# Kernel optimization log

Hardware: AMD Instinct MI355X
Metric: run time of the kernel (lower is better)

## Reference

```python
import jax, jax.numpy as jnp
import numpy as np

N = 8192        # nodes
D_IN = 512      # input features
H = 256         # hidden (GAT out_features)
D_OUT = 16      # output classes
K = 16          # num clusters/classes
LRELU_SLOPE = 0.2
MASK_FILL = -9e15
EDGE_P = 0.002  # sparsity of random adjacency


def setup_inputs() -> dict:
    key = jax.random.key(0)
    k1, k2, k3, k4, k5, k6 = jax.random.split(key, 6)
    x = jax.random.normal(k1, (N, D_IN), dtype=jnp.float32)
    # binary adjacency with self loops (module only tests adj > 0; support reused as propagation matrix)
    adj = (jax.random.uniform(k2, (N, N)) < EDGE_P).astype(jnp.float32)
    adj = jnp.maximum(adj, jnp.eye(N, dtype=jnp.float32))
    C_a = jax.random.normal(k3, (K, H), dtype=jnp.float32)
    # learned parameters (xavier-ish scale)
    W = jax.random.normal(k4, (D_IN, H), dtype=jnp.float32) * (1.414 * (2.0 / (D_IN + H)) ** 0.5)
    a = jax.random.normal(k5, (2 * H, 1), dtype=jnp.float32) * (1.414 * (2.0 / (2 * H + 1)) ** 0.5)
    W_gcn = jax.random.normal(k6, (H, D_OUT), dtype=jnp.float32)
    return {"x": x, "adj": adj, "C_a": C_a, "W": W, "a": a, "W_gcn": W_gcn}


def _clust_score(Z, C):
    # score[n,k] = exp(-||Z_n - C_k||) normalized over k (beta = 1)
    d = jnp.sqrt(((Z[:, None, :] - C[None, :, :]) ** 2).sum(-1))  # [N,K]
    s = jnp.exp(-d) + 1e-10
    return s / s.sum(axis=1, keepdims=True)


def reference(x, adj, C_a, W, a, W_gcn):
    h = W.shape[1]
    # --- GAT layer ---
    Wh = x @ W                                   # [N,H]
    Wh1 = Wh @ a[:h, :]                          # [N,1]
    Wh2 = Wh @ a[h:, :]                          # [N,1]
    e = jax.nn.leaky_relu(Wh1 + Wh2.T, LRELU_SLOPE)   # [N,N]
    att = jax.nn.softmax(jnp.where(adj > 0, e, MASK_FILL), axis=1)
    Z_0 = att @ Wh                               # h_prime, [N,H]
    gatoutput = jax.nn.elu(Z_0)
    # --- cluster score on detached Z_0 (update=False path) ---
    score = _clust_score(jax.lax.stop_gradient(Z_0), C_a)
    # --- GCN layer (B_1 = I, so Z_1 = F_1) ---
    F_1 = jax.nn.relu(adj @ (gatoutput @ W_gcn))  # [N,D_OUT]
    output = F_1
    Z_1 = F_1
    return (output, Z_1, Z_0, score)
```

## Files before the change

### kernel.cpp

```cpp
#include <hip/hip_runtime.h>
#include <hip/hip_bf16.h>

#define N_NODES 8192
#define D_IN    512
#define H       256
#define D_OUT   16
#define K_CL    16
#define MAXN    96

#define OUT_OFF 0
#define Z1_OFF  131072
#define Z0_OFF  262144
#define SC_OFF  2359296

typedef unsigned int   u32;
typedef unsigned short u16;
typedef short s16x8 __attribute__((ext_vector_type(8)));
typedef float f32x4 __attribute__((ext_vector_type(4)));

__device__ __forceinline__ float load_in(const void* p, int bf, size_t idx) {
    if (bf) { u32 w = ((const u16*)p)[idx]; return __uint_as_float(w << 16); }
    return ((const float*)p)[idx];
}
__device__ __forceinline__ void store_out(void* p, int bf, size_t idx, float v) {
    if (bf) ((__hip_bfloat16*)p)[idx] = __float2bfloat16(v);
    else    ((float*)p)[idx] = v;
}
__device__ __forceinline__ u16 f2bf(float v) {
    return (u16)__hip_bfloat16_raw(__float2bfloat16(v)).x;
}
__device__ __forceinline__ float bf2f(u16 b) { return __uint_as_float(((u32)b) << 16); }

__global__ void k_detect(const u32* __restrict__ adjw, int* __restrict__ flag) {
    int t = blockIdx.x * 256 + threadIdx.x;
    int hit = 0;
    #pragma unroll 4
    for (int i = 0; i < 64; i++)
        if (adjw[(size_t)t + (size_t)i * 16384] == 0x00003F80u) hit = 1;
    if (hit) atomicOr(flag, 1);
}

__global__ void k_prep(const void* av, const void* C_a, const void* Wgcn, const void* W,
                       const int* __restrict__ flag,
                       float* a_f, float* Ca_f, float* Wg_f,
                       u16* Wht, u16* Wlt) {
    int bf = *flag;
    int i = blockIdx.x * 256 + threadIdx.x;
    if (i < 512)        a_f[i]         = load_in(av,   bf, i);
    else if (i < 4608)  Ca_f[i - 512]  = load_in(C_a,  bf, i - 512);
    else if (i < 8704)  Wg_f[i - 4608] = load_in(Wgcn, bf, i - 4608);
    else if (i < 139776) {
        int j = i - 8704;
        int nn = j >> 9, kk = j & 511;
        size_t src = (size_t)kk * H + nn;
        if (bf) {
            Wht[j] = ((const u16*)W)[src];
            Wlt[j] = 0;
        } else {
            float w = ((const float*)W)[src];
            u16 hi = f2bf(w);
            Wht[j] = hi;
            Wlt[j] = f2bf(w - bf2f(hi));
        }
    }
}

__global__ __launch_bounds__(1024) void k_gemm_wh(
    const void* __restrict__ xraw,
    const u16* __restrict__ Wht, const u16* __restrict__ Wlt,
    const int* __restrict__ flag, float* __restrict__ Wh)
{
    int bf = *flag;
    int tid = threadIdx.x, wave = tid >> 6, lane = tid & 63;
    int m0 = blockIdx.x * 16, n0 = wave * 16;
    int quad = lane >> 4, lr = lane & 15;

    size_t boff = (size_t)(n0 + lr) * D_IN + quad * 8;
    const u16* bh = Wht + boff;
    f32x4 acc = {0.f, 0.f, 0.f, 0.f};

    if (bf) {
        const u16* ah = (const u16*)xraw + (size_t)(m0 + lr) * D_IN + quad * 8;
        #pragma unroll
        for (int k0 = 0; k0 < D_IN; k0 += 32) {
            s16x8 a = *(const s16x8*)(ah + k0);
            s16x8 b = *(const s16x8*)(bh + k0);
            acc = __builtin_amdgcn_mfma_f32_16x16x32_bf16(a, b, acc, 0, 0, 0);
        }
    } else {
        const float* af = (const float*)xraw + (size_t)(m0 + lr) * D_IN + quad * 8;
        const u16* bl = Wlt + boff;
        #pragma unroll
        for (int k0 = 0; k0 < D_IN; k0 += 32) {
            float4 f0 = *(const float4*)(af + k0);
            float4 f1 = *(const float4*)(af + k0 + 4);
            float v[8] = {f0.x, f0.y, f0.z, f0.w, f1.x, f1.y, f1.z, f1.w};
            s16x8 ahi, alo;
            #pragma unroll
            for (int i = 0; i < 8; i++) {
                u16 h = f2bf(v[i]);
                ahi[i] = (short)h;
                alo[i] = (short)f2bf(v[i] - bf2f(h));
            }
            s16x8 b  = *(const s16x8*)(bh + k0);
            s16x8 b2 = *(const s16x8*)(bl + k0);
            acc = __builtin_amdgcn_mfma_f32_16x16x32_bf16(ahi, b,  acc, 0, 0, 0);
            acc = __builtin_amdgcn_mfma_f32_16x16x32_bf16(ahi, b2, acc, 0, 0, 0);
            acc = __builtin_amdgcn_mfma_f32_16x16x32_bf16(alo, b,  acc, 0, 0, 0);
        }
    }
    float* cp = Wh + (size_t)(m0 + quad * 4) * H + n0 + lr;
    #pragma unroll
    for (int i = 0; i < 4; i++) cp[(size_t)i * H] = acc[i];
}

__global__ __launch_bounds__(256) void k_wh12(
    const float* __restrict__ Wh, const float* __restrict__ a_f,
    float* __restrict__ Wh1, float* __restrict__ Wh2)
{
    int tid = threadIdx.x;
    int wave = tid >> 6, lane = tid & 63;
    int n = blockIdx.x * 4 + wave;
    float4 v  = *(const float4*)(Wh + (size_t)n * H + lane * 4);
    float4 a1 = *(const float4*)(a_f + lane * 4);
    float4 a2 = *(const float4*)(a_f + H + lane * 4);
    float s1 = v.x*a1.x + v.y*a1.y + v.z*a1.z + v.w*a1.w;
    float s2 = v.x*a2.x + v.y*a2.y + v.z*a2.z + v.w*a2.w;
    #pragma unroll
    for (int off = 32; off; off >>= 1) {
        s1 += __shfl_xor(s1, off);
        s2 += __shfl_xor(s2, off);
    }
    if (lane == 0) { Wh1[n] = s1; Wh2[n] = s2; }
}

__global__ __launch_bounds__(256) void k_gat_row(
    const void* __restrict__ adjraw, const int* __restrict__ flag,
    const float* __restrict__ Wh,
    const float* __restrict__ Wh1, const float* __restrict__ Wh2,
    const float* __restrict__ Ca_f, const float* __restrict__ Wg_f,
    float* __restrict__ Gf,
    int* __restrict__ nbr_cnt, u16* __restrict__ nbr_idx,
    void* __restrict__ dout)
{
    const int n = blockIdx.x;
    const int tid = threadIdx.x;
    const int wave = tid >> 6, lane = tid & 63;
    const int bf = *flag;
    __shared__ int   s_cnt;
    __shared__ int   s_idx[MAXN];
    __shared__ float s_att[MAXN];
    __shared__ float s_z[H];
    __shared__ float s_g[H];
    __shared__ float s_red[256];
    __shared__ float s_sc[16];

    if (tid == 0) s_cnt = 0;
    __syncthreads();

    if (bf) {
        const u16* arow = (const u16*)adjraw + (size_t)n * N_NODES;
        #pragma unroll
        for (int it = 0; it < 4; it++) {
            int base = it * 2048 + tid * 8;
            uint4 raw = *(const uint4*)(arow + base);
            u32 rw[4] = {raw.x, raw.y, raw.z, raw.w};
            #pragma unroll
            for (int q = 0; q < 4; q++) {
                #pragma unroll
                for (int hh = 0; hh < 2; hh++) {
                    u32 u = (rw[q] >> (16 * hh)) & 0xFFFFu;
                    if (__uint_as_float(u << 16) > 0.f) {
                        int p = atomicAdd(&s_cnt, 1);
                        if (p < MAXN) s_idx[p] = base + q * 2 + hh;
                    }
                }
            }
        }
    } else {
        const float* arow = (const float*)adjraw + (size_t)n * N_NODES;
        #pragma unroll
        for (int it = 0; it < 8; it++) {
            int base = it * 1024 + tid * 4;
            float4 v = *(const float4*)(arow + base);
            float vv[4] = {v.x, v.y, v.z, v.w};
            #pragma unroll
            for (int q = 0; q < 4; q++) {
                if (vv[q] > 0.f) {
                    int p = atomicAdd(&s_cnt, 1);
                    if (p < MAXN) s_idx[p] = base + q;
                }
            }
        }
    }
    __syncthreads();
    const int cnt = min(s_cnt, MAXN);
    if (tid == 0) nbr_cnt[n] = cnt;
    if (tid < cnt) nbr_idx[(size_t)n * MAXN + tid] = (u16)s_idx[tid];

    if (wave == 0) {
        int t1 = lane, t2 = 64 + lane;
        float whn = Wh1[n];
        float e1 = -3e38f, e2 = -3e38f;
        if (t1 < cnt) { float v = whn + Wh2[s_idx[t1]]; e1 = v > 0.f ? v : 0.2f * v; }
        if (t2 < cnt) { float v = whn + Wh2[s_idx[t2]]; e2 = v > 0.f ? v : 0.2f * v; }
        float m = fmaxf(e1, e2);
        #pragma unroll
        for (int off = 32; off; off >>= 1) m = fmaxf(m, __shfl_xor(m, off));
        float x1 = (t1 < cnt) ? expf(e1 - m) : 0.f;
        float x2 = (t2 < cnt) ? expf(e2 - m) : 0.f;
        float s = x1 + x2;
        #pragma unroll
        for (int off = 32; off; off >>= 1) s += __shfl_xor(s, off);
        float inv = 1.f / s;
        if (t1 < cnt) s_att[t1] = x1 * inv;
        if (t2 < cnt) s_att[t2] = x2 * inv;
    }
    __syncthreads();

    float acc = 0.f;
    for (int t = 0; t < cnt; t++)
        acc += s_att[t] * Wh[(size_t)s_idx[t] * H + tid];
    s_z[tid] = acc;
    store_out(dout, bf, (size_t)Z0_OFF + (size_t)n * H + tid, acc);
    s_g[tid] = acc > 0.f ? acc : expf(acc) - 1.f;
    __syncthreads();

    {
        int k = tid & 15, hb = (tid >> 4) * 16;
        float p = 0.f;
        #pragma unroll
        for (int i = 0; i < 16; i++) {
            float d = s_z[hb + i] - Ca_f[(size_t)k * H + hb + i];
            p += d * d;
        }
        s_red[tid] = p;
    }
    __syncthreads();
    if (tid < 16) {
        float d2 = 0.f;
        #pragma unroll
        for (int q = 0; q < 16; q++) d2 += s_red[q * 16 + tid];
        s_sc[tid] = expf(-sqrtf(d2)) + 1e-10f;
    }
    __syncthreads();
    if (tid < 16) {
        float tot = 0.f;
        #pragma unroll
        for (int q = 0; q < 16; q++) tot += s_sc[q];
        store_out(dout, bf, (size_t)SC_OFF + (size_t)n * K_CL + tid, s_sc[tid] / tot);
    }
    {
        int o = tid & 15, hb = (tid >> 4) * 16;
        float p = 0.f;
        #pragma unroll
        for (int i = 0; i < 16; i++)
            p += s_g[hb + i] * Wg_f[(size_t)(hb + i) * D_OUT + o];
        s_red[tid] = p;
    }
    __syncthreads();
    if (tid < 16) {
        float g2 = 0.f;
        #pragma unroll
        for (int q = 0; q < 16; q++) g2 += s_red[q * 16 + tid];
        Gf[(size_t)n * D_OUT + tid] = g2;
    }
}

__global__ __launch_bounds__(256) void k_f1(
    const int* __restrict__ nbr_cnt, const u16* __restrict__ nbr_idx,
    const float* __restrict__ Gf, const int* __restrict__ flag,
    void* __restrict__ dout)
{
    int tid = threadIdx.x;
    int bf = *flag;
    int r = tid >> 4, o = tid & 15;
    int n = blockIdx.x * 16 + r;
    int cnt = nbr_cnt[n];
    const u16* idx = nbr_idx + (size_t)n * MAXN;
    float acc = 0.f;
    for (int t = 0; t < cnt; t++)
        acc += Gf[(size_t)idx[t] * D_OUT + o];
    acc = fmaxf(acc, 0.f);
    store_out(dout, bf, (size_t)OUT_OFF + (size_t)n * D_OUT + o, acc);
    store_out(dout, bf, (size_t)Z1_OFF  + (size_t)n * D_OUT + o, acc);
}

extern "C" void kernel_launch(void* const* d_in, const int* in_sizes, int n_in,
                              void* d_out, int out_size, void* d_ws, size_t ws_size,
                              hipStream_t stream) {
    const void* x    = d_in[0];
    const void* adj  = d_in[1];
    const void* C_a  = d_in[2];
    const void* W    = d_in[3];
    const void* av   = d_in[4];
    const void* Wgcn = d_in[5];

    char* wsp = (char*)d_ws;
    int*   flag = (int*)wsp;                   wsp += 256;
    float* Wh   = (float*)wsp;                 wsp += (size_t)N_NODES * H * 4;
    float* Wh1  = (float*)wsp;                 wsp += (size_t)N_NODES * 4;
    float* Wh2  = (float*)wsp;                 wsp += (size_t)N_NODES * 4;
    float* Gf   = (float*)wsp;                 wsp += (size_t)N_NODES * D_OUT * 4;
    int*   ncnt = (int*)wsp;                   wsp += (size_t)N_NODES * 4;
    u16*   nidx = (u16*)wsp;                   wsp += (size_t)N_NODES * MAXN * 2;
    float* a_f  = (float*)wsp;                 wsp += 2 * H * 4;
    float* Ca_f = (float*)wsp;                 wsp += (size_t)K_CL * H * 4;
    float* Wg_f = (float*)wsp;                 wsp += (size_t)H * D_OUT * 4;
    u16*   Wht  = (u16*)wsp;                   wsp += (size_t)H * D_IN * 2;
    u16*   Wlt  = (u16*)wsp;                   wsp += (size_t)H * D_IN * 2;

    hipMemsetAsync(flag, 0, sizeof(int), stream);
    k_detect <<<64, 256, 0, stream>>>((const u32*)adj, flag);
    k_prep   <<<546, 256, 0, stream>>>(av, C_a, Wgcn, W, flag, a_f, Ca_f, Wg_f, Wht, Wlt);
    k_gemm_wh<<<512, 1024, 0, stream>>>(x, Wht, Wlt, flag, Wh);
    k_wh12   <<<N_NODES / 4, 256, 0, stream>>>(Wh, a_f, Wh1, Wh2);
    k_gat_row<<<N_NODES, 256, 0, stream>>>(adj, flag, Wh, Wh1, Wh2, Ca_f, Wg_f,
                                           Gf, ncnt, nidx, d_out);
    k_f1     <<<N_NODES / 16, 256, 0, stream>>>(ncnt, nidx, Gf, flag, d_out);
}
```

Before: 475.6 us.

## Fuse all stages into one cooperative persistent kernel with grid syncs

Result: slower. 622.8 us (+31.0%).

```diff
diff --git a/kernel.cpp b/kernel.cpp
--- a/kernel.cpp
+++ b/kernel.cpp
@@ -1,5 +1,8 @@
 #include <hip/hip_runtime.h>
 #include <hip/hip_bf16.h>
+#include <hip/hip_cooperative_groups.h>
+
+namespace cg = cooperative_groups;
 
 #define N_NODES 8192
 #define D_IN    512
@@ -31,259 +34,252 @@
 }
 __device__ __forceinline__ float bf2f(u16 b) { return __uint_as_float(((u32)b) << 16); }
 
-__global__ void k_detect(const u32* __restrict__ adjw, int* __restrict__ flag) {
-    int t = blockIdx.x * 256 + threadIdx.x;
-    int hit = 0;
-    #pragma unroll 4
-    for (int i = 0; i < 64; i++)
-        if (adjw[(size_t)t + (size_t)i * 16384] == 0x00003F80u) hit = 1;
-    if (hit) atomicOr(flag, 1);
-}
-
-__global__ void k_prep(const void* av, const void* C_a, const void* Wgcn, const void* W,
-                       const int* __restrict__ flag,
-                       float* a_f, float* Ca_f, float* Wg_f,
-                       u16* Wht, u16* Wlt) {
-    int bf = *flag;
-    int i = blockIdx.x * 256 + threadIdx.x;
-    if (i < 512)        a_f[i]         = load_in(av,   bf, i);
-    else if (i < 4608)  Ca_f[i - 512]  = load_in(C_a,  bf, i - 512);
-    else if (i < 8704)  Wg_f[i - 4608] = load_in(Wgcn, bf, i - 4608);
-    else if (i < 139776) {
-        int j = i - 8704;
-        int nn = j >> 9, kk = j & 511;
-        size_t src = (size_t)kk * H + nn;
-        if (bf) {
-            Wht[j] = ((const u16*)W)[src];
-            Wlt[j] = 0;
-        } else {
-            float w = ((const float*)W)[src];
-            u16 hi = f2bf(w);
-            Wht[j] = hi;
-            Wlt[j] = f2bf(w - bf2f(hi));
-        }
-    }
-}
-
-__global__ __launch_bounds__(1024) void k_gemm_wh(
-    const void* __restrict__ xraw,
-    const u16* __restrict__ Wht, const u16* __restrict__ Wlt,
-    const int* __restrict__ flag, float* __restrict__ Wh)
-{
-    int bf = *flag;
-    int tid = threadIdx.x, wave = tid >> 6, lane = tid & 63;
-    int m0 = blockIdx.x * 16, n0 = wave * 16;
-    int quad = lane >> 4, lr = lane & 15;
-
-    size_t boff = (size_t)(n0 + lr) * D_IN + quad * 8;
-    const u16* bh = Wht + boff;
-    f32x4 acc = {0.f, 0.f, 0.f, 0.f};
-
-    if (bf) {
-        const u16* ah = (const u16*)xraw + (size_t)(m0 + lr) * D_IN + quad * 8;
-        #pragma unroll
-        for (int k0 = 0; k0 < D_IN; k0 += 32) {
-            s16x8 a = *(const s16x8*)(ah + k0);
-            s16x8 b = *(const s16x8*)(bh + k0);
-            acc = __builtin_amdgcn_mfma_f32_16x16x32_bf16(a, b, acc, 0, 0, 0);
-        }
-    } else {
-        const float* af = (const float*)xraw + (size_t)(m0 + lr) * D_IN + quad * 8;
-        const u16* bl = Wlt + boff;
-        #pragma unroll
-        for (int k0 = 0; k0 < D_IN; k0 += 32) {
-            float4 f0 = *(const float4*)(af + k0);
-            float4 f1 = *(const float4*)(af + k0 + 4);
-            float v[8] = {f0.x, f0.y, f0.z, f0.w, f1.x, f1.y, f1.z, f1.w};
-            s16x8 ahi, alo;
-            #pragma unroll
-            for (int i = 0; i < 8; i++) {
-                u16 h = f2bf(v[i]);
-                ahi[i] = (short)h;
-                alo[i] = (short)f2bf(v[i] - bf2f(h));
-            }
-            s16x8 b  = *(const s16x8*)(bh + k0);
-            s16x8 b2 = *(const s16x8*)(bl + k0);
-            acc = __builtin_amdgcn_mfma_f32_16x16x32_bf16(ahi, b,  acc, 0, 0, 0);
-            acc = __builtin_amdgcn_mfma_f32_16x16x32_bf16(ahi, b2, acc, 0, 0, 0);
-            acc = __builtin_amdgcn_mfma_f32_16x16x32_bf16(alo, b,  acc, 0, 0, 0);
-        }
-    }
-    float* cp = Wh + (size_t)(m0 + quad * 4) * H + n0 + lr;
-    #pragma unroll
-    for (int i = 0; i < 4; i++) cp[(size_t)i * H] = acc[i];
-}
-
-__global__ __launch_bounds__(256) void k_wh12(
-    const float* __restrict__ Wh, const float* __restrict__ a_f,
-    float* __restrict__ Wh1, float* __restrict__ Wh2)
-{
-    int tid = threadIdx.x;
-    int wave = tid >> 6, lane = tid & 63;
-    int n = blockIdx.x * 4 + wave;
-    float4 v  = *(const float4*)(Wh + (size_t)n * H + lane * 4);
-    float4 a1 = *(const float4*)(a_f + lane * 4);
-    float4 a2 = *(const float4*)(a_f + H + lane * 4);
-    float s1 = v.x*a1.x + v.y*a1.y + v.z*a1.z + v.w*a1.w;
-    float s2 = v.x*a2.x + v.y*a2.y + v.z*a2.z + v.w*a2.w;
-    #pragma unroll
-    for (int off = 32; off; off >>= 1) {
-        s1 += __shfl_xor(s1, off);
-        s2 += __shfl_xor(s2, off);
-    }
-    if (lane == 0) { Wh1[n] = s1; Wh2[n] = s2; }
-}
-
-__global__ __launch_bounds__(256) void k_gat_row(
-    const void* __restrict__ adjraw, const int* __restrict__ flag,
-    const float* __restrict__ Wh,
-    const float* __restrict__ Wh1, const float* __restrict__ Wh2,
-    const float* __restrict__ Ca_f, const float* __restrict__ Wg_f,
-    float* __restrict__ Gf,
-    int* __restrict__ nbr_cnt, u16* __restrict__ nbr_idx,
+__global__ __launch_bounds__(1024) void k_all(
+    const void* __restrict__ x, const void* __restrict__ adj,
+    const void* __restrict__ C_a, const void* __restrict__ W,
+    const void* __restrict__ av, const void* __restrict__ Wgcn,
+    int* __restrict__ flag,
+    float* __restrict__ Wh, float* __restrict__ Wh1, float* __restrict__ Wh2,
+    float* __restrict__ Gf, int* __restrict__ ncnt, u16* __restrict__ nidx,
+    float* __restrict__ a_f, float* __restrict__ Ca_f, float* __restrict__ Wg_f,
+    u16* __restrict__ Wht, u16* __restrict__ Wlt,
     void* __restrict__ dout)
 {
-    const int n = blockIdx.x;
+    cg::grid_group grid = cg::this_grid();
     const int tid = threadIdx.x;
-    const int wave = tid >> 6, lane = tid & 63;
+    const size_t gt = (size_t)blockIdx.x * 1024 + tid;
+
+    __shared__ int   s_cnt[4];
+    __shared__ int   s_idx[4][MAXN];
+    __shared__ float s_att[4][MAXN];
+    __shared__ float s_z[4][H];
+    __shared__ float s_g[4][H];
+    __shared__ float s_red[4][256];
+    __shared__ float s_sc[4][16];
+
+    {
+        uint4 v = ((const uint4*)adj)[gt];
+        if (v.x == 0x00003F80u || v.y == 0x00003F80u ||
+            v.z == 0x00003F80u || v.w == 0x00003F80u) atomicOr(flag, 1);
+        if (gt < N_NODES) { Wh1[gt] = 0.f; Wh2[gt] = 0.f; }
+    }
+    grid.sync();
+
     const int bf = *flag;
-    __shared__ int   s_cnt;
-    __shared__ int   s_idx[MAXN];
-    __shared__ float s_att[MAXN];
-    __shared__ float s_z[H];
-    __shared__ float s_g[H];
-    __shared__ float s_red[256];
-    __shared__ float s_sc[16];
-
-    if (tid == 0) s_cnt = 0;
-    __syncthreads();
-
-    if (bf) {
-        const u16* arow = (const u16*)adjraw + (size_t)n * N_NODES;
-        #pragma unroll
-        for (int it = 0; it < 4; it++) {
-            int base = it * 2048 + tid * 8;
-            uint4 raw = *(const uint4*)(arow + base);
-            u32 rw[4] = {raw.x, raw.y, raw.z, raw.w};
+
+    if (gt < 139776) {
+        int i = (int)gt;
+        if (i < 512)        a_f[i]         = load_in(av,   bf, i);
+        else if (i < 4608)  Ca_f[i - 512]  = load_in(C_a,  bf, i - 512);
+        else if (i < 8704)  Wg_f[i - 4608] = load_in(Wgcn, bf, i - 4608);
+        else {
+            int j = i - 8704;
+            int nn = j >> 9, kk = j & 511;
+            size_t src = (size_t)kk * H + nn;
+            if (bf) {
+                Wht[j] = ((const u16*)W)[src];
+                Wlt[j] = 0;
+            } else {
+                float w = ((const float*)W)[src];
+                u16 hi = f2bf(w);
+                Wht[j] = hi;
+                Wlt[j] = f2bf(w - bf2f(hi));
+            }
+        }
+    }
+    grid.sync();
+
+    {
+        int wave = tid >> 6, lane = tid & 63;
+        int quad = lane >> 4, lr = lane & 15;
+        int gw = blockIdx.x * 16 + wave;
+        for (int t = gw; t < 8192; t += 4096) {
+            int m0 = (t >> 4) * 16, n0 = (t & 15) * 16;
+            size_t boff = (size_t)(n0 + lr) * D_IN + quad * 8;
+            const u16* bh = Wht + boff;
+            f32x4 acc = {0.f, 0.f, 0.f, 0.f};
+            if (bf) {
+                const u16* ah = (const u16*)x + (size_t)(m0 + lr) * D_IN + quad * 8;
+                #pragma unroll
+                for (int k0 = 0; k0 < D_IN; k0 += 32) {
+                    s16x8 a = *(const s16x8*)(ah + k0);
+                    s16x8 b = *(const s16x8*)(bh + k0);
+                    acc = __builtin_amdgcn_mfma_f32_16x16x32_bf16(a, b, acc, 0, 0, 0);
+                }
+            } else {
+                const float* af = (const float*)x + (size_t)(m0 + lr) * D_IN + quad * 8;
+                const u16* bl = Wlt + boff;
+                #pragma unroll
+                for (int k0 = 0; k0 < D_IN; k0 += 32) {
+                    float4 f0 = *(const float4*)(af + k0);
+                    float4 f1 = *(const float4*)(af + k0 + 4);
+                    float v[8] = {f0.x, f0.y, f0.z, f0.w, f1.x, f1.y, f1.z, f1.w};
+                    s16x8 ahi, alo;
+                    #pragma unroll
+                    for (int i = 0; i < 8; i++) {
+                        u16 h = f2bf(v[i]);
+                        ahi[i] = (short)h;
+                        alo[i] = (short)f2bf(v[i] - bf2f(h));
+                    }
+                    s16x8 b  = *(const s16x8*)(bh + k0);
+                    s16x8 b2 = *(const s16x8*)(bl + k0);
+                    acc = __builtin_amdgcn_mfma_f32_16x16x32_bf16(ahi, b,  acc, 0, 0, 0);
+                    acc = __builtin_amdgcn_mfma_f32_16x16x32_bf16(ahi, b2, acc, 0, 0, 0);
+                    acc = __builtin_amdgcn_mfma_f32_16x16x32_bf16(alo, b,  acc, 0, 0, 0);
+                }
+            }
+            float* cp = Wh + (size_t)(m0 + quad * 4) * H + n0 + lr;
             #pragma unroll
-            for (int q = 0; q < 4; q++) {
-                #pragma unroll
-                for (int hh = 0; hh < 2; hh++) {
-                    u32 u = (rw[q] >> (16 * hh)) & 0xFFFFu;
-                    if (__uint_as_float(u << 16) > 0.f) {
-                        int p = atomicAdd(&s_cnt, 1);
-                        if (p < MAXN) s_idx[p] = base + q * 2 + hh;
+            for (int i = 0; i < 4; i++) cp[(size_t)i * H] = acc[i];
+            float a1v = a_f[n0 + lr], a2v = a_f[H + n0 + lr];
+            #pragma unroll
+            for (int i = 0; i < 4; i++) {
+                float p1 = acc[i] * a1v, p2 = acc[i] * a2v;
+                #pragma unroll
+                for (int off = 1; off < 16; off <<= 1) {
+                    p1 += __shfl_xor(p1, off);
+                    p2 += __shfl_xor(p2, off);
+                }
+                if (lr == 0) {
+                    atomicAdd(&Wh1[m0 + quad * 4 + i], p1);
+                    atomicAdd(&Wh2[m0 + quad * 4 + i], p2);
+                }
+            }
+        }
+    }
+    grid.sync();
+
+    {
+        const int g = tid >> 8, lt = tid & 255;
+        const int lane = lt & 63;
+        for (int it = 0; it < 8; it++) {
+            const int n = blockIdx.x * 32 + it * 4 + g;
+            if (lt == 0) s_cnt[g] = 0;
+            __syncthreads();
+
+            if (bf) {
+                const u16* arow = (const u16*)adj + (size_t)n * N_NODES;
+                #pragma unroll
+                for (int it2 = 0; it2 < 4; it2++) {
+                    int base = it2 * 2048 + lt * 8;
+                    uint4 raw = *(const uint4*)(arow + base);
+                    u32 rw[4] = {raw.x, raw.y, raw.z, raw.w};
+                    #pragma unroll
+                    for (int q = 0; q < 4; q++) {
+                        #pragma unroll
+                        for (int hh = 0; hh < 2; hh++) {
+                            u32 u = (rw[q] >> (16 * hh)) & 0xFFFFu;
+                            if (__uint_as_float(u << 16) > 0.f) {
+                                int p = atomicAdd(&s_cnt[g], 1);
+                                if (p < MAXN) s_idx[g][p] = base + q * 2 + hh;
+                            }
+                        }
                     }
                 }
-            }
+            } else {
+                const float* arow = (const float*)adj + (size_t)n * N_NODES;
+                #pragma unroll
+                for (int it2 = 0; it2 < 8; it2++) {
+                    int base = it2 * 1024 + lt * 4;
+                    float4 v = *(const float4*)(arow + base);
+                    float vv[4] = {v.x, v.y, v.z, v.w};
+                    #pragma unroll
+                    for (int q = 0; q < 4; q++) {
+                        if (vv[q] > 0.f) {
+                            int p = atomicAdd(&s_cnt[g], 1);
+                            if (p < MAXN) s_idx[g][p] = base + q;
+                        }
+                    }
+                }
+            }
+            __syncthreads();
+            const int cnt = min(s_cnt[g], MAXN);
+            if (lt == 0) ncnt[n] = cnt;
+            if (lt < cnt) nidx[(size_t)n * MAXN + lt] = (u16)s_idx[g][lt];
+
+            if (lt < 64) {
+                int t1 = lane, t2 = 64 + lane;
+                float whn = Wh1[n];
+                float e1 = -3e38f, e2 = -3e38f;
+                if (t1 < cnt) { float v = whn + Wh2[s_idx[g][t1]]; e1 = v > 0.f ? v : 0.2f * v; }
+                if (t2 < cnt) { float v = whn + Wh2[s_idx[g][t2]]; e2 = v > 0.f ? v : 0.2f * v; }
+                float m = fmaxf(e1, e2);
+                #pragma unroll
+                for (int off = 32; off; off >>= 1) m = fmaxf(m, __shfl_xor(m, off));
+                float x1 = (t1 < cnt) ? expf(e1 - m) : 0.f;
+                float x2 = (t2 < cnt) ? expf(e2 - m) : 0.f;
+                float s = x1 + x2;
+                #pragma unroll
+                for (int off = 32; off; off >>= 1) s += __shfl_xor(s, off);
+                float inv = 1.f / s;
+                if (t1 < cnt) s_att[g][t1] = x1 * inv;
+                if (t2 < cnt) s_att[g][t2] = x2 * inv;
+            }
+            __syncthreads();
+
+            float acc = 0.f;
+            for (int t = 0; t < cnt; t++)
+                acc += s_att[g][t] * Wh[(size_t)s_idx[g][t] * H + lt];
+            s_z[g][lt] = acc;
+            store_out(dout, bf, (size_t)Z0_OFF + (size_t)n * H + lt, acc);
+            s_g[g][lt] = acc > 0.f ? acc : expf(acc) - 1.f;
+            __syncthreads();
+
+            {
+                int k = lt & 15, hb = (lt >> 4) * 16;
+                float p = 0.f;
+                #pragma unroll
+                for (int i = 0; i < 16; i++) {
+                    float d = s_z[g][hb + i] - Ca_f[(size_t)k * H + hb + i];
+                    p += d * d;
+                }
+                s_red[g][lt] = p;
+            }
+            __syncthreads();
+            if (lt < 16) {
+                float d2 = 0.f;
+                #pragma unroll
+                for (int q = 0; q < 16; q++) d2 += s_red[g][q * 16 + lt];
+                s_sc[g][lt] = expf(-sqrtf(d2)) + 1e-10f;
+            }
+            __syncthreads();
+            if (lt < 16) {
+                float tot = 0.f;
+                #pragma unroll
+                for (int q = 0; q < 16; q++) tot += s_sc[g][q];
+                store_out(dout, bf, (size_t)SC_OFF + (size_t)n * K_CL + lt, s_sc[g][lt] / tot);
+            }
+            {
+                int o = lt & 15, hb = (lt >> 4) * 16;
+                float p = 0.f;
+                #pragma unroll
+                for (int i = 0; i < 16; i++)
+                    p += s_g[g][hb + i] * Wg_f[(size_t)(hb + i) * D_OUT + o];
+                s_red[g][lt] = p;
+            }
+            __syncthreads();
+            if (lt < 16) {
+                float g2 = 0.f;
+                #pragma unroll
+                for (int q = 0; q < 16; q++) g2 += s_red[g][q * 16 + lt];
+                Gf[(size_t)n * D_OUT + lt] = g2;
+            }
+            __syncthreads();
         }
-    } else {
-        const float* arow = (const float*)adjraw + (size_t)n * N_NODES;
-        #pragma unroll
-        for (int it = 0; it < 8; it++) {
-            int base = it * 1024 + tid * 4;
-            float4 v = *(const float4*)(arow + base);
-            float vv[4] = {v.x, v.y, v.z, v.w};
-            #pragma unroll
-            for (int q = 0; q < 4; q++) {
-                if (vv[q] > 0.f) {
-                    int p = atomicAdd(&s_cnt, 1);
-                    if (p < MAXN) s_idx[p] = base + q;
-                }
-            }
-        }
-    }
-    __syncthreads();
-    const int cnt = min(s_cnt, MAXN);
-    if (tid == 0) nbr_cnt[n] = cnt;
-    if (tid < cnt) nbr_idx[(size_t)n * MAXN + tid] = (u16)s_idx[tid];
-
-    if (wave == 0) {
-        int t1 = lane, t2 = 64 + lane;
-        float whn = Wh1[n];
-        float e1 = -3e38f, e2 = -3e38f;
-        if (t1 < cnt) { float v = whn + Wh2[s_idx[t1]]; e1 = v > 0.f ? v : 0.2f * v; }
-        if (t2 < cnt) { float v = whn + Wh2[s_idx[t2]]; e2 = v > 0.f ? v : 0.2f * v; }
-        float m = fmaxf(e1, e2);
-        #pragma unroll
-        for (int off = 32; off; off >>= 1) m = fmaxf(m, __shfl_xor(m, off));
-        float x1 = (t1 < cnt) ? expf(e1 - m) : 0.f;
-        float x2 = (t2 < cnt) ? expf(e2 - m) : 0.f;
-        float s = x1 + x2;
-        #pragma unroll
-        for (int off = 32; off; off >>= 1) s += __shfl_xor(s, off);
-        float inv = 1.f / s;
-        if (t1 < cnt) s_att[t1] = x1 * inv;
-        if (t2 < cnt) s_att[t2] = x2 * inv;
-    }
-    __syncthreads();
-
-    float acc = 0.f;
-    for (int t = 0; t < cnt; t++)
-        acc += s_att[t] * Wh[(size_t)s_idx[t] * H + tid];
-    s_z[tid] = acc;
-    store_out(dout, bf, (size_t)Z0_OFF + (size_t)n * H + tid, acc);
-    s_g[tid] = acc > 0.f ? acc : expf(acc) - 1.f;
-    __syncthreads();
-
-    {
-        int k = tid & 15, hb = (tid >> 4) * 16;
-        float p = 0.f;
-        #pragma unroll
-        for (int i = 0; i < 16; i++) {
-            float d = s_z[hb + i] - Ca_f[(size_t)k * H + hb + i];
-            p += d * d;
-        }
-        s_red[tid] = p;
-    }
-    __syncthreads();
-    if (tid < 16) {
-        float d2 = 0.f;
-        #pragma unroll
-        for (int q = 0; q < 16; q++) d2 += s_red[q * 16 + tid];
-        s_sc[tid] = expf(-sqrtf(d2)) + 1e-10f;
-    }
-    __syncthreads();
-    if (tid < 16) {
-        float tot = 0.f;
-        #pragma unroll
-        for (int q = 0; q < 16; q++) tot += s_sc[q];
-        store_out(dout, bf, (size_t)SC_OFF + (size_t)n * K_CL + tid, s_sc[tid] / tot);
-    }
-    {
-        int o = tid & 15, hb = (tid >> 4) * 16;
-        float p = 0.f;
-        #pragma unroll
-        for (int i = 0; i < 16; i++)
-            p += s_g[hb + i] * Wg_f[(size_t)(hb + i) * D_OUT + o];
-        s_red[tid] = p;
-    }
-    __syncthreads();
-    if (tid < 16) {
-        float g2 = 0.f;
-        #pragma unroll
-        for (int q = 0; q < 16; q++) g2 += s_red[q * 16 + tid];
-        Gf[(size_t)n * D_OUT + tid] = g2;
-    }
-}
-
-__global__ __launch_bounds__(256) void k_f1(
-    const int* __restrict__ nbr_cnt, const u16* __restrict__ nbr_idx,
-    const float* __restrict__ Gf, const int* __restrict__ flag,
-    void* __restrict__ dout)
-{
-    int tid = threadIdx.x;
-    int bf = *flag;
-    int r = tid >> 4, o = tid & 15;
-    int n = blockIdx.x * 16 + r;
-    int cnt = nbr_cnt[n];
-    const u16* idx = nbr_idx + (size_t)n * MAXN;
-    float acc = 0.f;
-    for (int t = 0; t < cnt; t++)
-        acc += Gf[(size_t)idx[t] * D_OUT + o];
-    acc = fmaxf(acc, 0.f);
-    store_out(dout, bf, (size_t)OUT_OFF + (size_t)n * D_OUT + o, acc);
-    store_out(dout, bf, (size_t)Z1_OFF  + (size_t)n * D_OUT + o, acc);
+    }
+    grid.sync();
+
+    if (gt < (size_t)N_NODES * D_OUT) {
+        int n = (int)(gt >> 4), o = (int)(gt & 15);
+        int cnt = ncnt[n];
+        const u16* idx = nidx + (size_t)n * MAXN;
+        float acc = 0.f;
+        for (int t = 0; t < cnt; t++)
+            acc += Gf[(size_t)idx[t] * D_OUT + o];
+        acc = fmaxf(acc, 0.f);
+        store_out(dout, bf, (size_t)OUT_OFF + gt, acc);
+        store_out(dout, bf, (size_t)Z1_OFF  + gt, acc);
+    }
 }
 
 extern "C" void kernel_launch(void* const* d_in, const int* in_sizes, int n_in,
@@ -311,11 +307,13 @@
     u16*   Wlt  = (u16*)wsp;                   wsp += (size_t)H * D_IN * 2;
 
     hipMemsetAsync(flag, 0, sizeof(int), stream);
-    k_detect <<<64, 256, 0, stream>>>((const u32*)adj, flag);
-    k_prep   <<<546, 256, 0, stream>>>(av, C_a, Wgcn, W, flag, a_f, Ca_f, Wg_f, Wht, Wlt);
-    k_gemm_wh<<<512, 1024, 0, stream>>>(x, Wht, Wlt, flag, Wh);
-    k_wh12   <<<N_NODES / 4, 256, 0, stream>>>(Wh, a_f, Wh1, Wh2);
-    k_gat_row<<<N_NODES, 256, 0, stream>>>(adj, flag, Wh, Wh1, Wh2, Ca_f, Wg_f,
-                                           Gf, ncnt, nidx, d_out);
-    k_f1     <<<N_NODES / 16, 256, 0, stream>>>(ncnt, nidx, Gf, flag, d_out);
-}
+
+    void* args[] = {
+        (void*)&x, (void*)&adj, (void*)&C_a, (void*)&W, (void*)&av, (void*)&Wgcn,
+        (void*)&flag, (void*)&Wh, (void*)&Wh1, (void*)&Wh2, (void*)&Gf,
+        (void*)&ncnt, (void*)&nidx, (void*)&a_f, (void*)&Ca_f, (void*)&Wg_f,
+        (void*)&Wht, (void*)&Wlt, (void*)&d_out
+    };
+    hipLaunchCooperativeKernel(reinterpret_cast<void*>(k_all),
+                               dim3(256), dim3(1024), args, 0, stream);
+}
```

## Co-schedule Wh GEMM with adjacency neighbor scan in one fused launch

Applied to the files above, without the earlier changes.

New measurement: 481.2 us. Within noise of the previous version (+1.2%).

```diff
diff --git a/kernel.cpp b/kernel.cpp
--- a/kernel.cpp
+++ b/kernel.cpp
@@ -12,6 +12,8 @@
 #define Z1_OFF  131072
 #define Z0_OFF  262144
 #define SC_OFF  2359296
+
+#define GEMM_BLOCKS 2048
 
 typedef unsigned int   u32;
 typedef unsigned short u16;
@@ -65,89 +67,131 @@
     }
 }
 
-__global__ __launch_bounds__(1024) void k_gemm_wh(
-    const void* __restrict__ xraw,
+__global__ __launch_bounds__(256) void k_big(
+    const void* __restrict__ x, const void* __restrict__ adj,
     const u16* __restrict__ Wht, const u16* __restrict__ Wlt,
-    const int* __restrict__ flag, float* __restrict__ Wh)
+    const float* __restrict__ a_f, const int* __restrict__ flag,
+    float* __restrict__ Wh, float* __restrict__ Wh1, float* __restrict__ Wh2,
+    int* __restrict__ ncnt, u16* __restrict__ nidx)
 {
-    int bf = *flag;
-    int tid = threadIdx.x, wave = tid >> 6, lane = tid & 63;
-    int m0 = blockIdx.x * 16, n0 = wave * 16;
-    int quad = lane >> 4, lr = lane & 15;
-
-    size_t boff = (size_t)(n0 + lr) * D_IN + quad * 8;
-    const u16* bh = Wht + boff;
-    f32x4 acc = {0.f, 0.f, 0.f, 0.f};
-
-    if (bf) {
-        const u16* ah = (const u16*)xraw + (size_t)(m0 + lr) * D_IN + quad * 8;
-        #pragma unroll
-        for (int k0 = 0; k0 < D_IN; k0 += 32) {
-            s16x8 a = *(const s16x8*)(ah + k0);
-            s16x8 b = *(const s16x8*)(bh + k0);
-            acc = __builtin_amdgcn_mfma_f32_16x16x32_bf16(a, b, acc, 0, 0, 0);
+    const int bf = *flag;
+    const int tid = threadIdx.x;
+
+    if (blockIdx.x < GEMM_BLOCKS) {
+        int wave = tid >> 6, lane = tid & 63;
+        int quad = lane >> 4, lr = lane & 15;
+        int t = blockIdx.x * 4 + wave;
+        int m0 = (t >> 4) * 16, n0 = (t & 15) * 16;
+        size_t boff = (size_t)(n0 + lr) * D_IN + quad * 8;
+        const u16* bh = Wht + boff;
+        f32x4 acc = {0.f, 0.f, 0.f, 0.f};
+        if (bf) {
+            const u16* ah = (const u16*)x + (size_t)(m0 + lr) * D_IN + quad * 8;
+            #pragma unroll
+            for (int k0 = 0; k0 < D_IN; k0 += 32) {
+                s16x8 a = *(const s16x8*)(ah + k0);
+                s16x8 b = *(const s16x8*)(bh + k0);
+                acc = __builtin_amdgcn_mfma_f32_16x16x32_bf16(a, b, acc, 0, 0, 0);
+            }
+        } else {
+            const float* af = (const float*)x + (size_t)(m0 + lr) * D_IN + quad * 8;
+            const u16* bl = Wlt + boff;
+            #pragma unroll
+            for (int k0 = 0; k0 < D_IN; k0 += 32) {
+                float4 f0 = *(const float4*)(af + k0);
+                float4 f1 = *(const float4*)(af + k0 + 4);
+                float v[8] = {f0.x, f0.y, f0.z, f0.w, f1.x, f1.y, f1.z, f1.w};
+                s16x8 ahi, alo;
+                #pragma unroll
+                for (int i = 0; i < 8; i++) {
+                    u16 h = f2bf(v[i]);
+                    ahi[i] = (short)h;
+                    alo[i] = (short)f2bf(v[i] - bf2f(h));
+                }
+                s16x8 b  = *(const s16x8*)(bh + k0);
+                s16x8 b2 = *(const s16x8*)(bl + k0);
+                acc = __builtin_amdgcn_mfma_f32_16x16x32_bf16(ahi, b,  acc, 0, 0, 0);
+                acc = __builtin_amdgcn_mfma_f32_16x16x32_bf16(ahi, b2, acc, 0, 0, 0);
+                acc = __builtin_amdgcn_mfma_f32_16x16x32_bf16(alo, b,  acc, 0, 0, 0);
+            }
+        }
+        float* cp = Wh + (size_t)(m0 + quad * 4) * H + n0 + lr;
+        #pragma unroll
+        for (int i = 0; i < 4; i++) cp[(size_t)i * H] = acc[i];
+        float a1v = a_f[n0 + lr], a2v = a_f[H + n0 + lr];
+        #pragma unroll
+        for (int i = 0; i < 4; i++) {
+            float p1 = acc[i] * a1v, p2 = acc[i] * a2v;
+            #pragma unroll
+            for (int off = 1; off < 16; off <<= 1) {
+                p1 += __shfl_xor(p1, off);
+                p2 += __shfl_xor(p2, off);
+            }
+            if (lr == 0) {
+                atomicAdd(&Wh1[m0 + quad * 4 + i], p1);
+                atomicAdd(&Wh2[m0 + quad * 4 + i], p2);
+            }
         }
     } else {
-        const float* af = (const float*)xraw + (size_t)(m0 + lr) * D_IN + quad * 8;
-        const u16* bl = Wlt + boff;
-        #pragma unroll
-        for (int k0 = 0; k0 < D_IN; k0 += 32) {
-            float4 f0 = *(const float4*)(af + k0);
-            float4 f1 = *(const float4*)(af + k0 + 4);
-            float v[8] = {f0.x, f0.y, f0.z, f0.w, f1.x, f1.y, f1.z, f1.w};
-            s16x8 ahi, alo;
-            #pragma unroll
-            for (int i = 0; i < 8; i++) {
-                u16 h = f2bf(v[i]);
-                ahi[i] = (short)h;
-                alo[i] = (short)f2bf(v[i] - bf2f(h));
-            }
-            s16x8 b  = *(const s16x8*)(bh + k0);
-            s16x8 b2 = *(const s16x8*)(bl + k0);
-            acc = __builtin_amdgcn_mfma_f32_16x16x32_bf16(ahi, b,  acc, 0, 0, 0);
-            acc = __builtin_amdgcn_mfma_f32_16x16x32_bf16(ahi, b2, acc, 0, 0, 0);
-            acc = __builtin_amdgcn_mfma_f32_16x16x32_bf16(alo, b,  acc, 0, 0, 0);
-        }
-    }
-    float* cp = Wh + (size_t)(m0 + quad * 4) * H + n0 + lr;
-    #pragma unroll
-    for (int i = 0; i < 4; i++) cp[(size_t)i * H] = acc[i];
-}
-
-__global__ __launch_bounds__(256) void k_wh12(
-    const float* __restrict__ Wh, const float* __restrict__ a_f,
-    float* __restrict__ Wh1, float* __restrict__ Wh2)
-{
-    int tid = threadIdx.x;
-    int wave = tid >> 6, lane = tid & 63;
-    int n = blockIdx.x * 4 + wave;
-    float4 v  = *(const float4*)(Wh + (size_t)n * H + lane * 4);
-    float4 a1 = *(const float4*)(a_f + lane * 4);
-    float4 a2 = *(const float4*)(a_f + H + lane * 4);
-    float s1 = v.x*a1.x + v.y*a1.y + v.z*a1.z + v.w*a1.w;
-    float s2 = v.x*a2.x + v.y*a2.y + v.z*a2.z + v.w*a2.w;
-    #pragma unroll
-    for (int off = 32; off; off >>= 1) {
-        s1 += __shfl_xor(s1, off);
-        s2 += __shfl_xor(s2, off);
-    }
-    if (lane == 0) { Wh1[n] = s1; Wh2[n] = s2; }
-}
-
-__global__ __launch_bounds__(256) void k_gat_row(
-    const void* __restrict__ adjraw, const int* __restrict__ flag,
+        const int n = blockIdx.x - GEMM_BLOCKS;
+        __shared__ int s_cnt;
+        __shared__ int s_idx[MAXN];
+        if (tid == 0) s_cnt = 0;
+        __syncthreads();
+        if (bf) {
+            const u16* arow = (const u16*)adj + (size_t)n * N_NODES;
+            #pragma unroll
+            for (int it = 0; it < 4; it++) {
+                int base = it * 2048 + tid * 8;
+                uint4 raw = *(const uint4*)(arow + base);
+                u32 rw[4] = {raw.x, raw.y, raw.z, raw.w};
+                #pragma unroll
+                for (int q = 0; q < 4; q++) {
+                    #pragma unroll
+                    for (int hh = 0; hh < 2; hh++) {
+                        u32 u = (rw[q] >> (16 * hh)) & 0xFFFFu;
+                        if (__uint_as_float(u << 16) > 0.f) {
+                            int p = atomicAdd(&s_cnt, 1);
+                            if (p < MAXN) s_idx[p] = base + q * 2 + hh;
+                        }
+                    }
+                }
+            }
+        } else {
+            const float* arow = (const float*)adj + (size_t)n * N_NODES;
+            #pragma unroll
+            for (int it = 0; it < 8; it++) {
+                int base = it * 1024 + tid * 4;
+                float4 v = *(const float4*)(arow + base);
+                float vv[4] = {v.x, v.y, v.z, v.w};
+                #pragma unroll
+                for (int q = 0; q < 4; q++) {
+                    if (vv[q] > 0.f) {
+                        int p = atomicAdd(&s_cnt, 1);
+                        if (p < MAXN) s_idx[p] = base + q;
+                    }
+                }
+            }
+        }
+        __syncthreads();
+        const int cnt = min(s_cnt, MAXN);
+        if (tid == 0) ncnt[n] = cnt;
+        if (tid < cnt) nidx[(size_t)n * MAXN + tid] = (u16)s_idx[tid];
+    }
+}
+
+__global__ __launch_bounds__(256) void k_gat2(
+    const int* __restrict__ flag,
     const float* __restrict__ Wh,
     const float* __restrict__ Wh1, const float* __restrict__ Wh2,
     const float* __restrict__ Ca_f, const float* __restrict__ Wg_f,
-    float* __restrict__ Gf,
-    int* __restrict__ nbr_cnt, u16* __restrict__ nbr_idx,
-    void* __restrict__ dout)
+    const int* __restrict__ ncnt, const u16* __restrict__ nidx,
+    float* __restrict__ Gf, void* __restrict__ dout)
 {
     const int n = blockIdx.x;
     const int tid = threadIdx.x;
     const int wave = tid >> 6, lane = tid & 63;
     const int bf = *flag;
-    __shared__ int   s_cnt;
     __shared__ int   s_idx[MAXN];
     __shared__ float s_att[MAXN];
     __shared__ float s_z[H];
@@ -155,48 +199,9 @@
     __shared__ float s_red[256];
     __shared__ float s_sc[16];
 
-    if (tid == 0) s_cnt = 0;
-    __syncthreads();
-
-    if (bf) {
-        const u16* arow = (const u16*)adjraw + (size_t)n * N_NODES;
-        #pragma unroll
-        for (int it = 0; it < 4; it++) {
-            int base = it * 2048 + tid * 8;
-            uint4 raw = *(const uint4*)(arow + base);
-            u32 rw[4] = {raw.x, raw.y, raw.z, raw.w};
-            #pragma unroll
-            for (int q = 0; q < 4; q++) {
-                #pragma unroll
-                for (int hh = 0; hh < 2; hh++) {
-                    u32 u = (rw[q] >> (16 * hh)) & 0xFFFFu;
-                    if (__uint_as_float(u << 16) > 0.f) {
-                        int p = atomicAdd(&s_cnt, 1);
-                        if (p < MAXN) s_idx[p] = base + q * 2 + hh;
-                    }
-                }
-            }
-        }
-    } else {
-        const float* arow = (const float*)adjraw + (size_t)n * N_NODES;
-        #pragma unroll
-        for (int it = 0; it < 8; it++) {
-            int base = it * 1024 + tid * 4;
-            float4 v = *(const float4*)(arow + base);
-            float vv[4] = {v.x, v.y, v.z, v.w};
-            #pragma unroll
-            for (int q = 0; q < 4; q++) {
-                if (vv[q] > 0.f) {
-                    int p = atomicAdd(&s_cnt, 1);
-                    if (p < MAXN) s_idx[p] = base + q;
-                }
-            }
-        }
-    }
-    __syncthreads();
-    const int cnt = min(s_cnt, MAXN);
-    if (tid == 0) nbr_cnt[n] = cnt;
-    if (tid < cnt) nbr_idx[(size_t)n * MAXN + tid] = (u16)s_idx[tid];
+    const int cnt = ncnt[n];
+    if (tid < cnt) s_idx[tid] = nidx[(size_t)n * MAXN + tid];
+    __syncthreads();
 
     if (wave == 0) {
         int t1 = lane, t2 = 64 + lane;
@@ -268,7 +273,7 @@
 }
 
 __global__ __launch_bounds__(256) void k_f1(
-    const int* __restrict__ nbr_cnt, const u16* __restrict__ nbr_idx,
+    const int* __restrict__ ncnt, const u16* __restrict__ nidx,
     const float* __restrict__ Gf, const int* __restrict__ flag,
     void* __restrict__ dout)
 {
@@ -276,8 +281,8 @@
     int bf = *flag;
     int r = tid >> 4, o = tid & 15;
     int n = blockIdx.x * 16 + r;
-    int cnt = nbr_cnt[n];
-    const u16* idx = nbr_idx + (size_t)n * MAXN;
+    int cnt = ncnt[n];
+    const u16* idx = nidx + (size_t)n * MAXN;
     float acc = 0.f;
     for (int t = 0; t < cnt; t++)
         acc += Gf[(size_t)idx[t] * D_OUT + o];
@@ -298,9 +303,9 @@
 
     char* wsp = (char*)d_ws;
     int*   flag = (int*)wsp;                   wsp += 256;
-    float* Wh   = (float*)wsp;                 wsp += (size_t)N_NODES * H * 4;
     float* Wh1  = (float*)wsp;                 wsp += (size_t)N_NODES * 4;
     float* Wh2  = (float*)wsp;                 wsp += (size_t)N_NODES * 4;
+    float* Wh   = (float*)wsp;                 wsp += (size_t)N_NODES * H * 4;
     float* Gf   = (float*)wsp;                 wsp += (size_t)N_NODES * D_OUT * 4;
     int*   ncnt = (int*)wsp;                   wsp += (size_t)N_NODES * 4;
     u16*   nidx = (u16*)wsp;                   wsp += (size_t)N_NODES * MAXN * 2;
@@ -310,12 +315,12 @@
     u16*   Wht  = (u16*)wsp;                   wsp += (size_t)H * D_IN * 2;
     u16*   Wlt  = (u16*)wsp;                   wsp += (size_t)H * D_IN * 2;
 
-    hipMemsetAsync(flag, 0, sizeof(int), stream);
-    k_detect <<<64, 256, 0, stream>>>((const u32*)adj, flag);
-    k_prep   <<<546, 256, 0, stream>>>(av, C_a, Wgcn, W, flag, a_f, Ca_f, Wg_f, Wht, Wlt);
-    k_gemm_wh<<<512, 1024, 0, stream>>>(x, Wht, Wlt, flag, Wh);
-    k_wh12   <<<N_NODES / 4, 256, 0, stream>>>(Wh, a_f, Wh1, Wh2);
-    k_gat_row<<<N_NODES, 256, 0, stream>>>(adj, flag, Wh, Wh1, Wh2, Ca_f, Wg_f,
-                                           Gf, ncnt, nidx, d_out);
-    k_f1     <<<N_NODES / 16, 256, 0, stream>>>(ncnt, nidx, Gf, flag, d_out);
-}
+    hipMemsetAsync(flag, 0, 256 + (size_t)N_NODES * 8, stream);
+    k_detect<<<64, 256, 0, stream>>>((const u32*)adj, flag);
+    k_prep  <<<546, 256, 0, stream>>>(av, C_a, Wgcn, W, flag, a_f, Ca_f, Wg_f, Wht, Wlt);
+    k_big   <<<GEMM_BLOCKS + N_NODES, 256, 0, stream>>>(x, adj, Wht, Wlt, a_f, flag,
+                                                        Wh, Wh1, Wh2, ncnt, nidx);
+    k_gat2  <<<N_NODES, 256, 0, stream>>>(flag, Wh, Wh1, Wh2, Ca_f, Wg_f, ncnt, nidx,
+                                          Gf, d_out);
+    k_f1    <<<N_NODES / 16, 256, 0, stream>>>(ncnt, nidx, Gf, flag, d_out);
+}
```
